# Optimization experiments

Measured on AMD Instinct MI355X. Metric: run time of the kernel, lower is better.

## Reference

```python
import jax, jax.numpy as jnp
import numpy as np

B, C, W, H = 4, 512, 64, 64
C8 = C // 8


def setup_inputs() -> dict:
    key = jax.random.key(0)
    ks = jax.random.split(key, 8)
    s = 1.0 / np.sqrt(C)  # conv2d 1x1 fan-in init scale
    return {
        "x": jax.random.normal(ks[0], (B, C, W, H), jnp.float32),
        "y": jax.random.normal(ks[1], (B, C, W, H), jnp.float32),
        "wq": jax.random.uniform(ks[2], (C8, C), jnp.float32, -s, s),
        "bq": jax.random.uniform(ks[3], (C8,), jnp.float32, -s, s),
        "wk": jax.random.uniform(ks[4], (C8, C), jnp.float32, -s, s),
        "bk": jax.random.uniform(ks[5], (C8,), jnp.float32, -s, s),
        "wv": jax.random.uniform(ks[6], (C, C), jnp.float32, -s, s),
        "bv": jax.random.uniform(ks[7], (C,), jnp.float32, -s, s),
        "gamma": jnp.zeros((1,), jnp.float32),
    }


def reference(x, y, wq, bq, wk, bk, wv, bv, gamma):
    b, c, w, h = x.shape
    n = w * h
    yf = y.reshape(b, c, n)        # [B, C, N]
    xf = x.reshape(b, c, n)        # [B, C, N]
    # 1x1 convs are channel-wise linear maps
    q = jnp.einsum('oc,bcn->bno', wq, yf) + bq              # [B, N, C8]
    k = jnp.einsum('oc,bcn->bon', wk, yf) + bk[:, None]      # [B, C8, N]
    energy = jnp.einsum('bno,bom->bnm', q, k)                # [B, N, N], no scaling (as in source)
    attention = jax.nn.softmax(energy, axis=2)
    v = jnp.einsum('oc,bcn->bon', wv, xf) + bv[:, None]      # [B, C, N]
    # out[b,c,m] = sum_n v[b,c,n] * attention[b,m,n]  (bmm with attention^T)
    out = jnp.einsum('bcn,bmn->bcm', v, attention).reshape(b, c, w, h)
    out = gamma[0] * out + x
    return (out, attention)
```

## Files before the change

kernel.cpp:

```cpp
#include <hip/hip_runtime.h>


#define BB 4
#define CC 512
#define NN 4096
#define C8V 64

typedef __bf16 bf16x8 __attribute__((ext_vector_type(8)));
typedef float f32x4 __attribute__((ext_vector_type(4)));
typedef float f32x4v __attribute__((ext_vector_type(4)));
typedef unsigned short u16x8 __attribute__((ext_vector_type(8)));

#if __has_builtin(__builtin_amdgcn_exp2f)
#define EXP2(x) __builtin_amdgcn_exp2f(x)
#else
#define EXP2(x) exp2f(x)
#endif

#define MFMA16(a, b, c) __builtin_amdgcn_mfma_f32_16x16x32_bf16((a), (b), (c), 0, 0, 0)

__device__ __forceinline__ unsigned short f2b(float f) {
  union { float f; unsigned u; } x; x.f = f;
  unsigned u = x.u;
  u += 0x7fffu + ((u >> 16) & 1u);
  return (unsigned short)(u >> 16);
}

__device__ __forceinline__ float b2f(unsigned short s) {
  union { unsigned u; float f; } x; x.u = ((unsigned)s) << 16;
  return x.f;
}

__device__ __forceinline__ bf16x8 ldb8(const unsigned short* p) {
  return *reinterpret_cast<const bf16x8*>(p);
}

__global__ __launch_bounds__(256) void k_cvt_w(
    const float* __restrict__ wq, const float* __restrict__ wk, const float* __restrict__ wv,
    unsigned short* __restrict__ wqb, unsigned short* __restrict__ wkb, unsigned short* __restrict__ wvb) {
  int i = blockIdx.x * 256 + threadIdx.x;
  if (i < 32768)        wqb[i] = f2b(wq[i]);
  else if (i < 65536)   wkb[i - 32768] = f2b(wk[i - 32768]);
  else if (i < 327680)  wvb[i - 65536] = f2b(wv[i - 65536]);
}

__global__ __launch_bounds__(256) void k_projqk(
    const float* __restrict__ y,
    const unsigned short* __restrict__ wqb, const unsigned short* __restrict__ wkb,
    const float* __restrict__ bq, const float* __restrict__ bk,
    unsigned short* __restrict__ q, unsigned short* __restrict__ ktp) {
  __shared__ unsigned short ytile[64][130];
  int b = blockIdx.y, n0 = blockIdx.x * 64;
  int t = threadIdx.x, w = t >> 6, l = t & 63, lr = l & 15, lk = l >> 4;
  const float* yb = y + (size_t)b * CC * NN;

  f32x4 qacc[4] = {}, kacc[4] = {};
  for (int slab = 0; slab < 4; slab++) {
    int cs = slab * 128;
#pragma unroll
    for (int r = 0; r < 8; r++) {
      int idx = t + r * 256, c = idx >> 4, n4 = (idx & 15) * 4;
      f32x4v v4 = *reinterpret_cast<const f32x4v*>(&yb[(size_t)(cs + c) * NN + n0 + n4]);
      ytile[n4 + 0][c] = f2b(v4.x); ytile[n4 + 1][c] = f2b(v4.y);
      ytile[n4 + 2][c] = f2b(v4.z); ytile[n4 + 3][c] = f2b(v4.w);
    }
    __syncthreads();
#pragma unroll
    for (int ks = 0; ks < 4; ks++) {
      bf16x8 a = *reinterpret_cast<const bf16x8*>(&ytile[w * 16 + lr][ks * 32 + lk * 8]);
      int cgl = cs + ks * 32 + lk * 8;
#pragma unroll
      for (int cg = 0; cg < 4; cg++) {
        qacc[cg] = MFMA16(a, ldb8(wqb + (size_t)(cg * 16 + lr) * CC + cgl), qacc[cg]);
        kacc[cg] = MFMA16(a, ldb8(wkb + (size_t)(cg * 16 + lr) * CC + cgl), kacc[cg]);
      }
    }
    __syncthreads();
  }
#pragma unroll
  for (int cg = 0; cg < 4; cg++) {
    int o = cg * 16 + lr;
    float bqv = bq[o], bkv = bk[o];
#pragma unroll
    for (int i = 0; i < 4; i++) {
      int n = n0 + w * 16 + lk * 4 + i;
      q[(size_t)(b * NN + n) * C8V + o] = f2b((qacc[cg][i] + bqv) * 1.44269504088896f);
      ktp[((size_t)(b * 256 + (n >> 4)) * 2 + (o >> 5)) * 512 + (n & 15) * 32 + (o & 31)] =
          f2b(kacc[cg][i] + bkv);
    }
  }
}

__global__ __launch_bounds__(512) void k_projv(
    const float* __restrict__ x, const unsigned short* __restrict__ wvb,
    const float* __restrict__ bv, unsigned short* __restrict__ vp) {
  __shared__ unsigned short xtile[64][130];
  int b = blockIdx.y, n0 = blockIdx.x * 64;
  int t = threadIdx.x, w = t >> 6, l = t & 63, lr = l & 15, lk = l >> 4;
  const float* xb = x + (size_t)b * CC * NN;
  int c0w = w * 64;

  f32x4 acc[4][4] = {};
  for (int slab = 0; slab < 4; slab++) {
    int cs = slab * 128;
#pragma unroll
    for (int r = 0; r < 4; r++) {
      int idx = t + r * 512, c = idx >> 4, n4 = (idx & 15) * 4;
      f32x4v v4 = *reinterpret_cast<const f32x4v*>(&xb[(size_t)(cs + c) * NN + n0 + n4]);
      xtile[n4 + 0][c] = f2b(v4.x); xtile[n4 + 1][c] = f2b(v4.y);
      xtile[n4 + 2][c] = f2b(v4.z); xtile[n4 + 3][c] = f2b(v4.w);
    }
    __syncthreads();
#pragma unroll
    for (int ks = 0; ks < 4; ks++) {
      bf16x8 bfr[4];
#pragma unroll
      for (int cg = 0; cg < 4; cg++)
        bfr[cg] = *reinterpret_cast<const bf16x8*>(&xtile[cg * 16 + lr][ks * 32 + lk * 8]);
#pragma unroll
      for (int rg = 0; rg < 4; rg++) {
        bf16x8 a = ldb8(wvb + (size_t)(c0w + rg * 16 + lr) * CC + cs + ks * 32 + lk * 8);
#pragma unroll
        for (int cg = 0; cg < 4; cg++)
          acc[rg][cg] = MFMA16(a, bfr[cg], acc[rg][cg]);
      }
    }
    __syncthreads();
  }
#pragma unroll
  for (int rg = 0; rg < 4; rg++)
#pragma unroll
    for (int i = 0; i < 4; i++) {
      int c = c0w + rg * 16 + lk * 4 + i;
      float bias = bv[c];
#pragma unroll
      for (int cg = 0; cg < 4; cg++) {
        int n = n0 + cg * 16 + lr;
        vp[((size_t)(b * 64 + (n >> 6)) * 2 + ((n >> 5) & 1)) * 16384 + c * 32 + (n & 31)] =
            f2b(acc[rg][cg][i] + bias);
      }
    }
}

__global__ __launch_bounds__(512) void k_sminv(const unsigned short* __restrict__ q,
                                               const unsigned short* __restrict__ ktp,
                                               float* __restrict__ invp) {
  __shared__ float psum[8][16];
  int b = blockIdx.y;
  int w = threadIdx.x >> 6, l = threadIdx.x & 63;
  int rg = w >> 2, cq = w & 3;
  int r0 = blockIdx.x * 32 + rg * 16;
  int lr = l & 15, lk = l >> 4;
  const unsigned short* qp = q + (size_t)(b * NN + r0 + lr) * C8V + lk * 8;
  bf16x8 aq0 = ldb8(qp);
  bf16x8 aq1 = ldb8(qp + 32);
  int jt0 = cq * 16;

  float lsum[4] = {0.f, 0.f, 0.f, 0.f};
  for (int jt = jt0; jt < jt0 + 16; jt++) {
    f32x4 acc[4] = {};
#pragma unroll
    for (int cg = 0; cg < 4; cg++) {
      size_t base = ((size_t)(b * 256 + jt * 4 + cg) * 2) * 512 + lr * 32 + lk * 8;
      acc[cg] = MFMA16(aq0, ldb8(ktp + base), acc[cg]);
      acc[cg] = MFMA16(aq1, ldb8(ktp + base + 512), acc[cg]);
    }
#pragma unroll
    for (int i = 0; i < 4; i++)
      lsum[i] += (EXP2(acc[0][i]) + EXP2(acc[1][i])) + (EXP2(acc[2][i]) + EXP2(acc[3][i]));
  }
#pragma unroll
  for (int i = 0; i < 4; i++) {
#pragma unroll
    for (int mm = 1; mm < 16; mm <<= 1) lsum[i] += __shfl_xor(lsum[i], mm);
  }
  if (lr == 0) {
#pragma unroll
    for (int i = 0; i < 4; i++) psum[w][lk * 4 + i] = lsum[i];
  }
  __syncthreads();
  if (cq == 0 && lr == 0) {
#pragma unroll
    for (int i = 0; i < 4; i++) {
      int rr = lk * 4 + i;
      float s = psum[rg * 4 + 0][rr] + psum[rg * 4 + 1][rr] +
                psum[rg * 4 + 2][rr] + psum[rg * 4 + 3][rr];
      invp[(size_t)b * NN + r0 + rr] = 1.0f / s;
    }
  }
}

__global__ __launch_bounds__(512, 2) void k_fused(const unsigned short* __restrict__ q,
                                                  const unsigned short* __restrict__ ktp,
                                                  const unsigned short* __restrict__ vp,
                                                  const float* __restrict__ invp,
                                                  const float* __restrict__ x,
                                                  const float* __restrict__ gamma,
                                                  float* __restrict__ out,
                                                  float* __restrict__ att) {
  __shared__ unsigned short smP[2][64 * 64];

  int bid = blockIdx.x;
  int b = (bid & 7) >> 1;
  int m0 = ((bid >> 3) * 2 + (bid & 1)) * 64;
  int t = threadIdx.x, w = t >> 6, l = t & 63, lr = l & 15, lk = l >> 4;
  int rg = w >> 1, nh = w & 1;
  int c0w = w * 64;
  int mrow = t >> 3, col8 = t & 7;

  float* ab = att + (size_t)b * NN * NN;

  const unsigned short* qp = q + (size_t)(b * NN + m0 + rg * 16 + lr) * C8V + lk * 8;
  bf16x8 aq0 = ldb8(qp), aq1 = ldb8(qp + 32);
  f32x4v invv = *reinterpret_cast<const f32x4v*>(&invp[(size_t)b * NN + m0 + rg * 16 + lk * 4]);

#define LDKT(D, JT)                                                            \
  _Pragma("unroll")                                                            \
  for (int cg = 0; cg < 2; cg++) {                                             \
    size_t base = ((size_t)(b * 256 + (JT) * 4 + nh * 2 + cg) * 2) * 512 +     \
                  lr * 32 + lk * 8;                                            \
    D[cg * 2] = ldb8(ktp + base);                                              \
    D[cg * 2 + 1] = ldb8(ktp + base + 512);                                    \
  }

#define LDV(D, JT)                                                             \
  _Pragma("unroll")                                                            \
  for (int rg2 = 0; rg2 < 4; rg2++) {                                          \
    size_t vbase = ((size_t)(b * 64 + (JT)) * 2) * 16384 +                     \
                   (c0w + rg2 * 16 + lr) * 32 + lk * 8;                        \
    D[rg2 * 2] = ldb8(vp + vbase);                                             \
    D[rg2 * 2 + 1] = ldb8(vp + vbase + 16384);                                 \
  }

#define QKSM(KT, BUF)                                                          \
  {                                                                            \
    char* pbuf = reinterpret_cast<char*>(&smP[BUF][0]);                        \
    _Pragma("unroll")                                                          \
    for (int cg = 0; cg < 2; cg++) {                                           \
      f32x4 z = {};                                                            \
      z = MFMA16(aq0, KT[cg * 2], z);                                          \
      z = MFMA16(aq1, KT[cg * 2 + 1], z);                                      \
      int nl = nh * 32 + cg * 16 + lr;                                         \
      _Pragma("unroll")                                                        \
      for (int i = 0; i < 4; i++) {                                            \
        int ml = rg * 16 + lk * 4 + i;                                         \
        float p = EXP2(z[i]) * invv[i];                                        \
        *reinterpret_cast<unsigned short*>(                                    \
            pbuf + ml * 128 + ((nl * 2) ^ ((ml & 7) << 4))) = f2b(p);          \
      }                                                                        \
    }                                                                          \
  }

#define ATTST(BUF, JT)                                                         \
  {                                                                            \
    const char* pr = reinterpret_cast<const char*>(&smP[BUF][0]);              \
    u16x8 raw = *reinterpret_cast<const u16x8*>(                               \
        pr + mrow * 128 + ((col8 * 16) ^ ((mrow & 7) << 4)));                  \
    f32x4v lo, hi;                                                             \
    lo.x = b2f(raw[0]); lo.y = b2f(raw[1]); lo.z = b2f(raw[2]);                \
    lo.w = b2f(raw[3]); hi.x = b2f(raw[4]); hi.y = b2f(raw[5]);                \
    hi.z = b2f(raw[6]); hi.w = b2f(raw[7]);                                    \
    float* dst = &ab[(size_t)(m0 + mrow) * NN + (JT) * 64 + col8 * 8];         \
    *reinterpret_cast<f32x4v*>(dst) = lo;                                      \
    *reinterpret_cast<f32x4v*>(dst + 4) = hi;                                  \
  }

#define PV(VR, BUF)                                                            \
  {                                                                            \
    const char* pr = reinterpret_cast<const char*>(&smP[BUF][0]);              \
    __builtin_amdgcn_s_setprio(1);                                             \
    _Pragma("unroll")                                                          \
    for (int ks = 0; ks < 2; ks++) {                                           \
      bf16x8 bfr[4];                                                           \
      _Pragma("unroll")                                                        \
      for (int cg = 0; cg < 4; cg++) {                                         \
        int mr = cg * 16 + lr;                                                 \
        bfr[cg] = *reinterpret_cast<const bf16x8*>(                            \
            pr + mr * 128 + ((ks * 64 + lk * 16) ^ ((mr & 7) << 4)));          \
      }                                                                        \
      _Pragma("unroll")                                                        \
      for (int rg2 = 0; rg2 < 4; rg2++)                                        \
        _Pragma("unroll")                                                      \
        for (int cg = 0; cg < 4; cg++)                                         \
          acc[rg2][cg] = MFMA16(VR[rg2 * 2 + ks], bfr[cg], acc[rg2][cg]);      \
    }                                                                          \
    __builtin_amdgcn_s_setprio(0);                                             \
  }

#define SB() __builtin_amdgcn_sched_barrier(0);

#define SYNC_NODRAIN()                                   \
  asm volatile("s_waitcnt lgkmcnt(0)" ::: "memory");     \
  __builtin_amdgcn_s_barrier();                          \
  __builtin_amdgcn_sched_barrier(0);

  f32x4 acc[4][4] = {};
  bf16x8 ktA[4], ktB[4];
  bf16x8 vA[8], vB[8];

  LDKT(ktA, 0);
  LDV(vA, 0);
  QKSM(ktA, 0);
  LDKT(ktB, 1);
  SYNC_NODRAIN();

#define BODY(G, KTF, VN, KTC, VC, CUR)                                         \
  {                                                                            \
    int g = (G);                                                               \
    if (g < 62) LDKT(KTF, g + 2);                             \
    if (g < 63) LDV(VN, g + 1);                                                \
    SB();                                                                      \
    ATTST(CUR, g);                                     \
    SB();                                                                      \
    if (g < 63) QKSM(KTC, (CUR) ^ 1);                \
    PV(VC, CUR);                                                               \
    SYNC_NODRAIN();                                                            \
  }

  for (int g2 = 0; g2 < 64; g2 += 2) {
    BODY(g2,     ktA, vB, ktB, vA, 0);
    BODY(g2 + 1, ktB, vA, ktA, vB, 1);
  }
#undef LDKT
#undef LDV
#undef QKSM
#undef ATTST
#undef PV
#undef SB
#undef SYNC_NODRAIN
#undef BODY

  float gm = gamma[0];
  const float* xb = x + (size_t)b * CC * NN;
  float* ob = out + (size_t)b * CC * NN;
#pragma unroll
  for (int rg2 = 0; rg2 < 4; rg2++)
#pragma unroll
    for (int i = 0; i < 4; i++) {
      int row = c0w + rg2 * 16 + lk * 4 + i;
#pragma unroll
      for (int cg = 0; cg < 4; cg++) {
        int col = m0 + cg * 16 + lr;
        size_t off = (size_t)row * NN + col;
        float xv = __builtin_nontemporal_load(&xb[off]);
        ob[off] = gm * acc[rg2][cg][i] + xv;
      }
    }
}

extern "C" void kernel_launch(void* const* d_in, const int* in_sizes, int n_in,
                              void* d_out, int out_size, void* d_ws, size_t ws_size,
                              hipStream_t stream) {
  const float* x  = (const float*)d_in[0];
  const float* y  = (const float*)d_in[1];
  const float* wq = (const float*)d_in[2];
  const float* bq = (const float*)d_in[3];
  const float* wk = (const float*)d_in[4];
  const float* bk = (const float*)d_in[5];
  const float* wv = (const float*)d_in[6];
  const float* bv = (const float*)d_in[7];
  const float* gamma = (const float*)d_in[8];

  float* out = (float*)d_out;
  float* att = out + (size_t)BB * CC * NN;

  char* ws = (char*)d_ws;
  unsigned short* q   = (unsigned short*)(ws);
  unsigned short* ktp = (unsigned short*)(ws + 2097152);
  unsigned short* vp  = (unsigned short*)(ws + 4194304);
  unsigned short* wqb = (unsigned short*)(ws + 20971520);
  unsigned short* wkb = (unsigned short*)(ws + 21037056);
  unsigned short* wvb = (unsigned short*)(ws + 21102592);
  float*          inv = (float*)(ws + 21626880);
  if (ws_size < 21692416u) return;

  k_cvt_w<<<1280, 256, 0, stream>>>(wq, wk, wv, wqb, wkb, wvb);
  k_projqk<<<dim3(64, 4), 256, 0, stream>>>(y, wqb, wkb, bq, bk, q, ktp);
  k_projv<<<dim3(64, 4), 512, 0, stream>>>(x, wvb, bv, vp);
  k_sminv<<<dim3(128, 4), 512, 0, stream>>>(q, ktp, inv);
  k_fused<<<256, 512, 0, stream>>>(q, ktp, vp, inv, x, gamma, out, att);
}
```

Measured before the change: 259.6 us.

## Fuse softmax row-sum pass into the fused attention kernel

Removes the separate k_sminv launch and computes each row's softmax denominator inside k_fused with a first QK^T sweep over all key tiles, reduced across lanes and the two column-half waves via shared memory. This drops one kernel launch plus the inverse-sum round trip through global memory. In exchange, each k_fused block now recomputes the full QK^T for its rows before the main loop, on a grid of only 256 blocks, so that prepass gets less parallelism than the 512-block standalone kernel had.

```diff
diff --git a/kernel.cpp b/kernel.cpp
--- a/kernel.cpp
+++ b/kernel.cpp
@@ -142,63 +142,15 @@
     }
 }
 
-__global__ __launch_bounds__(512) void k_sminv(const unsigned short* __restrict__ q,
-                                               const unsigned short* __restrict__ ktp,
-                                               float* __restrict__ invp) {
-  __shared__ float psum[8][16];
-  int b = blockIdx.y;
-  int w = threadIdx.x >> 6, l = threadIdx.x & 63;
-  int rg = w >> 2, cq = w & 3;
-  int r0 = blockIdx.x * 32 + rg * 16;
-  int lr = l & 15, lk = l >> 4;
-  const unsigned short* qp = q + (size_t)(b * NN + r0 + lr) * C8V + lk * 8;
-  bf16x8 aq0 = ldb8(qp);
-  bf16x8 aq1 = ldb8(qp + 32);
-  int jt0 = cq * 16;
-
-  float lsum[4] = {0.f, 0.f, 0.f, 0.f};
-  for (int jt = jt0; jt < jt0 + 16; jt++) {
-    f32x4 acc[4] = {};
-#pragma unroll
-    for (int cg = 0; cg < 4; cg++) {
-      size_t base = ((size_t)(b * 256 + jt * 4 + cg) * 2) * 512 + lr * 32 + lk * 8;
-      acc[cg] = MFMA16(aq0, ldb8(ktp + base), acc[cg]);
-      acc[cg] = MFMA16(aq1, ldb8(ktp + base + 512), acc[cg]);
-    }
-#pragma unroll
-    for (int i = 0; i < 4; i++)
-      lsum[i] += (EXP2(acc[0][i]) + EXP2(acc[1][i])) + (EXP2(acc[2][i]) + EXP2(acc[3][i]));
-  }
-#pragma unroll
-  for (int i = 0; i < 4; i++) {
-#pragma unroll
-    for (int mm = 1; mm < 16; mm <<= 1) lsum[i] += __shfl_xor(lsum[i], mm);
-  }
-  if (lr == 0) {
-#pragma unroll
-    for (int i = 0; i < 4; i++) psum[w][lk * 4 + i] = lsum[i];
-  }
-  __syncthreads();
-  if (cq == 0 && lr == 0) {
-#pragma unroll
-    for (int i = 0; i < 4; i++) {
-      int rr = lk * 4 + i;
-      float s = psum[rg * 4 + 0][rr] + psum[rg * 4 + 1][rr] +
-                psum[rg * 4 + 2][rr] + psum[rg * 4 + 3][rr];
-      invp[(size_t)b * NN + r0 + rr] = 1.0f / s;
-    }
-  }
-}
-
 __global__ __launch_bounds__(512, 2) void k_fused(const unsigned short* __restrict__ q,
                                                   const unsigned short* __restrict__ ktp,
                                                   const unsigned short* __restrict__ vp,
-                                                  const float* __restrict__ invp,
                                                   const float* __restrict__ x,
                                                   const float* __restrict__ gamma,
                                                   float* __restrict__ out,
                                                   float* __restrict__ att) {
   __shared__ unsigned short smP[2][64 * 64];
+  __shared__ float psum[8][16];
 
   int bid = blockIdx.x;
   int b = (bid & 7) >> 1;
@@ -212,7 +164,34 @@
 
   const unsigned short* qp = q + (size_t)(b * NN + m0 + rg * 16 + lr) * C8V + lk * 8;
   bf16x8 aq0 = ldb8(qp), aq1 = ldb8(qp + 32);
-  f32x4v invv = *reinterpret_cast<const f32x4v*>(&invp[(size_t)b * NN + m0 + rg * 16 + lk * 4]);
+
+  float lsum[4] = {0.f, 0.f, 0.f, 0.f};
+  for (int jt = 0; jt < 64; jt++) {
+    f32x4 acc2[2] = {};
+#pragma unroll
+    for (int cg = 0; cg < 2; cg++) {
+      size_t base = ((size_t)(b * 256 + jt * 4 + nh * 2 + cg) * 2) * 512 + lr * 32 + lk * 8;
+      acc2[cg] = MFMA16(aq0, ldb8(ktp + base), acc2[cg]);
+      acc2[cg] = MFMA16(aq1, ldb8(ktp + base + 512), acc2[cg]);
+    }
+#pragma unroll
+    for (int i = 0; i < 4; i++)
+      lsum[i] += EXP2(acc2[0][i]) + EXP2(acc2[1][i]);
+  }
+#pragma unroll
+  for (int i = 0; i < 4; i++) {
+#pragma unroll
+    for (int mm = 1; mm < 16; mm <<= 1) lsum[i] += __shfl_xor(lsum[i], mm);
+  }
+  if (lr == 0) {
+#pragma unroll
+    for (int i = 0; i < 4; i++) psum[w][lk * 4 + i] = lsum[i];
+  }
+  __syncthreads();
+  f32x4v invv;
+#pragma unroll
+  for (int i = 0; i < 4; i++)
+    invv[i] = 1.0f / (psum[rg * 2][lk * 4 + i] + psum[rg * 2 + 1][lk * 4 + i]);
 
 #define LDKT(D, JT)                                                            \
   _Pragma("unroll")                                                            \
@@ -371,12 +350,10 @@
   unsigned short* wqb = (unsigned short*)(ws + 20971520);
   unsigned short* wkb = (unsigned short*)(ws + 21037056);
   unsigned short* wvb = (unsigned short*)(ws + 21102592);
-  float*          inv = (float*)(ws + 21626880);
-  if (ws_size < 21692416u) return;
+  if (ws_size < 21626880u) return;
 
   k_cvt_w<<<1280, 256, 0, stream>>>(wq, wk, wv, wqb, wkb, wvb);
   k_projqk<<<dim3(64, 4), 256, 0, stream>>>(y, wqb, wkb, bq, bk, q, ktp);
   k_projv<<<dim3(64, 4), 512, 0, stream>>>(x, wvb, bv, vp);
-  k_sminv<<<dim3(128, 4), 512, 0, stream>>>(q, ktp, inv);
-  k_fused<<<256, 512, 0, stream>>>(q, ktp, vp, inv, x, gamma, out, att);
-}
+  k_fused<<<256, 512, 0, stream>>>(q, ktp, vp, x, gamma, out, att);
+}
```

New measurement: 257.6 us. About the same (-0.8%).
